# Performance work log

Hardware: AMD Instinct MI355X
Metric: run time of the kernel (lower is better)

The kernel has to match this reference:

```python
import jax, jax.numpy as jnp
import numpy as np

EMBED_DIM = 1024
BLOCK = 2048
HEAD = 64
BATCH = 4


def setup_inputs() -> dict:
    key = jax.random.key(0)
    k0, k1, k2, k3 = jax.random.split(key, 4)
    tokens = jax.random.normal(k0, (BATCH, BLOCK, EMBED_DIM), dtype=jnp.float32)
    # torch Linear(embed_dim, head_size, bias=False): init ~ U(-1/sqrt(in), 1/sqrt(in)).
    s = 1.0 / np.sqrt(EMBED_DIM)
    Wq = jax.random.uniform(k1, (EMBED_DIM, HEAD), jnp.float32, -s, s)
    Wk = jax.random.uniform(k2, (EMBED_DIM, HEAD), jnp.float32, -s, s)
    Wv = jax.random.uniform(k3, (EMBED_DIM, HEAD), jnp.float32, -s, s)
    return {"tokens": tokens, "Wq": Wq, "Wk": Wk, "Wv": Wv}


def reference(tokens, Wq, Wk, Wv):
    B, S, E = tokens.shape
    q = jnp.einsum('bse,eh->bsh', tokens, Wq)
    k = jnp.einsum('bse,eh->bsh', tokens, Wk)
    v = jnp.einsum('bse,eh->bsh', tokens, Wv)
    # NOTE: module scales by embed_dim**-0.5 (not head_size).
    wei = jnp.einsum('bqh,bkh->bqk', q, k) * (E ** -0.5)
    causal = jnp.tril(jnp.ones((S, S), dtype=bool))  # tril_mask[:block,:block]
    wei = jnp.where(causal, wei, -1e9)
    wei = jax.nn.softmax(wei, axis=-1)
    # dropout(p=0.3) is identity in eval mode (deterministic reference)
    return jnp.einsum('bqk,bkh->bqh', wei, v)
```

## Files before the change

### kernel.cpp

```cpp
#include <hip/hip_runtime.h>
#include <stdint.h>


typedef __bf16 bf16_t;
typedef __bf16 bf16x8 __attribute__((ext_vector_type(8)));
typedef __bf16 bf16x4 __attribute__((ext_vector_type(4)));
typedef float floatx4 __attribute__((ext_vector_type(4)));

#define MFMA16(a, b, c) __builtin_amdgcn_mfma_f32_16x16x32_bf16((a), (b), (c), 0, 0, 0)

static constexpr float kQScale = 0.04508422002778f;
#define NEG_BIG (-3.0e38f)

__device__ inline bf16x4 cvt4(float4 f) {
  bf16x4 v;
  v[0] = (bf16_t)f.x; v[1] = (bf16_t)f.y; v[2] = (bf16_t)f.z; v[3] = (bf16_t)f.w;
  return v;
}

__global__ __launch_bounds__(256) void wt_kernel(const float* __restrict__ Wq,
                                                 const float* __restrict__ Wk,
                                                 const float* __restrict__ Wv,
                                                 bf16_t* __restrict__ Bp) {
  const int tid = blockIdx.x * 256 + threadIdx.x;
  const int j = tid & 7;
  const int lane = (tid >> 3) & 63;
  const int ks = (tid >> 9) & 31;
  const int nt = tid >> 14;
  const int m = nt >> 2, n4 = nt & 3;
  const int h = n4 * 16 + (lane & 15);
  const int e = ks * 32 + ((lane >> 4) << 3) + j;
  const float* W = (m == 0) ? Wq : ((m == 1) ? Wk : Wv);
  float v = W[e * 64 + h];
  if (m == 0) v *= kQScale;
  Bp[tid] = (bf16_t)v;
}

__global__ __launch_bounds__(256) void proj_kernel(const float* __restrict__ tok,
                                                   const bf16_t* __restrict__ Bp,
                                                   bf16_t* __restrict__ qw,
                                                   bf16_t* __restrict__ kw,
                                                   bf16_t* __restrict__ vw) {
  __shared__ bf16_t As[2][16][264];
  const int tx = threadIdx.x;
  const int wave = tx >> 6, lane = tx & 63;
  const int lanelo = lane & 15, quad = lane >> 4;
  const int grow = blockIdx.x * 16;
  const int b = grow >> 11;
  const int t = (grow & 2047) >> 4;

  const float* tokbase = tok + (grow + wave) * 1024 + lane * 4;

  floatx4 acc[3];
#pragma unroll
  for (int i = 0; i < 3; i++) acc[i] = (floatx4){0.f, 0.f, 0.f, 0.f};

  const bf16_t* bp[3];
#pragma unroll
  for (int j = 0; j < 3; j++)
    bp[j] = Bp + (wave * 3 + j) * 16384 + lane * 8;

  float4 tb[4];
#pragma unroll
  for (int r = 0; r < 4; r++) tb[r] = *(const float4*)(tokbase + r * 4096);
#pragma unroll
  for (int r = 0; r < 4; r++)
    *(bf16x4*)&As[0][r * 4 + wave][lane * 4] = cvt4(tb[r]);
  __syncthreads();

  for (int c = 0; c < 4; c++) {
    if (c < 3) {
#pragma unroll
      for (int r = 0; r < 4; r++)
        tb[r] = *(const float4*)(tokbase + r * 4096 + (c + 1) * 256);
    }
    const bf16_t* ab = &As[c & 1][lanelo][quad * 8];
#pragma unroll
    for (int ks = 0; ks < 8; ks++) {
      const bf16x8 af = *(const bf16x8*)(ab + ks * 32);
#pragma unroll
      for (int j = 0; j < 3; j++) {
        const bf16x8 bfr = *(const bf16x8*)(bp[j] + (c * 8 + ks) * 512);
        acc[j] = MFMA16(af, bfr, acc[j]);
      }
    }
    if (c < 3) {
#pragma unroll
      for (int r = 0; r < 4; r++)
        *(bf16x4*)&As[(c + 1) & 1][r * 4 + wave][lane * 4] = cvt4(tb[r]);
    }
    __syncthreads();
  }

#pragma unroll
  for (int j = 0; j < 3; j++) {
    const int nt = wave * 3 + j;
    const int n4 = nt & 3, mtx = nt >> 2;
    const int h = n4 * 16 + lanelo;
    if (mtx < 2) {
      bf16_t* dst = (mtx == 0) ? qw : kw;
      const int ds = h >> 5;
      const int base = (((b * 128 + t) * 2 + ds) * 64 + (((h & 31) >> 3) << 4)) * 8 + (h & 7);
#pragma unroll
      for (int r = 0; r < 4; r++)
        dst[base + (quad * 4 + r) * 8] = (bf16_t)acc[j][r];
    } else {
#pragma unroll
      for (int r = 0; r < 4; r++) {
        const int ss = t * 16 + quad * 4 + r;
        const int c6 = ss >> 6, k6 = ss & 63;
        const int pos = ((k6 & 15) << 2) | (k6 >> 4);
        const int hh = pos >> 5, qv = (pos >> 3) & 3, jj = pos & 7;
        vw[((((b * 32 + c6) * 2 + hh) * 4 + n4) * 64 + qv * 16 + lanelo) * 8 + jj] =
            (bf16_t)acc[j][r];
      }
    }
  }
}

__global__ __launch_bounds__(512, 4) void attn_kernel(const bf16_t* __restrict__ qw,
                                                      const bf16_t* __restrict__ kw,
                                                      const bf16_t* __restrict__ vw,
                                                      float* __restrict__ out) {
  __shared__ float Ol[8][16][68];
  __shared__ float Ll[8][16];
  __shared__ bf16_t Pl[8][16 * 72];

  const int wave = threadIdx.x >> 6;
  const int lane = threadIdx.x & 63;
  const int lanelo = lane & 15;
  const int quad = lane >> 4;

  const int b = blockIdx.x & 3;
  const int t = 127 - (blockIdx.x >> 2);
  const int qbase = t * 16;
  const int grow = b * 2048 + qbase;

  const bf16_t* qp = qw + ((b * 128 + t) * 128 + lane) * 8;
  const bf16x8 qa0 = *(const bf16x8*)qp;
  const bf16x8 qa1 = *(const bf16x8*)(qp + 512);

  bf16x8 ones;
#pragma unroll
  for (int j = 0; j < 8; j++) ones[j] = (bf16_t)1.0f;

  floatx4 O[4];
#pragma unroll
  for (int i = 0; i < 4; i++) O[i] = (floatx4){0.f, 0.f, 0.f, 0.f};
  floatx4 lacc = (floatx4){0.f, 0.f, 0.f, 0.f};

  const int nch = (qbase + 16 + 63) >> 6;
  const int row0 = qbase + quad * 4;
  bf16_t* pw = &Pl[wave][0];
  const bf16_t* kb = kw + b * 131072 + lane * 8;
  const bf16_t* vb = vw + b * 131072 + lane * 8;

  for (int c = wave; c < nch; c += 8) {
    const int cb = c * 64;
    floatx4 s[4];
    const floatx4 z = (floatx4){0.f, 0.f, 0.f, 0.f};
#pragma unroll
    for (int sub = 0; sub < 4; sub++) {
      const bf16_t* kp = kb + (c * 4 + sub) * 1024;
      s[sub] = MFMA16(qa0, *(const bf16x8*)kp, z);
      s[sub] = MFMA16(qa1, *(const bf16x8*)(kp + 512), s[sub]);
    }

    if (cb + 63 > qbase) {
#pragma unroll
      for (int sub = 0; sub < 4; sub++) {
        const int key0 = cb + sub * 16 + lanelo;
#pragma unroll
        for (int r = 0; r < 4; r++)
          if (key0 > row0 + r) s[sub][r] = NEG_BIG;
      }
    }

    float p[4][4];
#pragma unroll
    for (int sub = 0; sub < 4; sub++)
#pragma unroll
      for (int r = 0; r < 4; r++)
        p[sub][r] = __builtin_amdgcn_exp2f(s[sub][r]);

    __builtin_amdgcn_wave_barrier();
#pragma unroll
    for (int r = 0; r < 4; r++) {
      bf16x4 pk;
      pk[0] = (bf16_t)p[0][r]; pk[1] = (bf16_t)p[1][r];
      pk[2] = (bf16_t)p[2][r]; pk[3] = (bf16_t)p[3][r];
      *(bf16x4*)&pw[(quad * 4 + r) * 72 + lanelo * 4] = pk;
    }
    __builtin_amdgcn_wave_barrier();
    const bf16_t* prd = pw + lanelo * 72 + quad * 8;
    const bf16x8 pa0 = *(const bf16x8*)prd;
    const bf16x8 pa1 = *(const bf16x8*)(prd + 32);
    __builtin_amdgcn_wave_barrier();

    const bf16_t* vp = vb + c * 4096;
#pragma unroll
    for (int dt = 0; dt < 4; dt++) {
      O[dt] = MFMA16(pa0, *(const bf16x8*)(vp + dt * 512), O[dt]);
      O[dt] = MFMA16(pa1, *(const bf16x8*)(vp + 2048 + dt * 512), O[dt]);
    }
    lacc = MFMA16(pa0, ones, lacc);
    lacc = MFMA16(pa1, ones, lacc);
  }

#pragma unroll
  for (int dt = 0; dt < 4; dt++)
#pragma unroll
    for (int r = 0; r < 4; r++)
      Ol[wave][quad * 4 + r][dt * 16 + lanelo] = O[dt][r];
  if (lanelo == 0) {
#pragma unroll
    for (int r = 0; r < 4; r++) Ll[wave][quad * 4 + r] = lacc[r];
  }
  __syncthreads();

#pragma unroll
  for (int o = threadIdx.x; o < 1024; o += 512) {
    const int row = o >> 6, d = o & 63;
    float L = 0.f, acc = 0.f;
#pragma unroll
    for (int w = 0; w < 8; w++) {
      L += Ll[w][row];
      acc += Ol[w][row][d];
    }
    out[(grow + row) * 64 + d] = acc / L;
  }
}

extern "C" void kernel_launch(void* const* d_in, const int* in_sizes, int n_in,
                              void* d_out, int out_size, void* d_ws, size_t ws_size,
                              hipStream_t stream) {
  const float* tokens = (const float*)d_in[0];
  const float* Wq = (const float*)d_in[1];
  const float* Wk = (const float*)d_in[2];
  const float* Wv = (const float*)d_in[3];
  float* out = (float*)d_out;

  char* ws = (char*)d_ws;
  if (ws_size < 3538944) return;
  bf16_t* Bp = (bf16_t*)ws;
  bf16_t* qw = (bf16_t*)(ws + 393216);
  bf16_t* kw = (bf16_t*)(ws + 393216 + 1048576);
  bf16_t* vw = (bf16_t*)(ws + 393216 + 2097152);

  hipLaunchKernelGGL(wt_kernel, dim3(768), dim3(256), 0, stream, Wq, Wk, Wv, Bp);
  hipLaunchKernelGGL(proj_kernel, dim3(512), dim3(256), 0, stream, tokens, Bp, qw, kw, vw);
  hipLaunchKernelGGL(attn_kernel, dim3(512), dim3(512), 0, stream, qw, kw, vw, out);
}
```

Baseline: 98.23 us.

## Transpose attention MFMAs to keep P in registers and stage projection stores via LDS

The attention kernel swaps the MFMA operand order so the score tile comes out transposed (keys along registers, queries along lanes). The exponentiated probabilities can then be packed straight into the B operand of the PV MFMA, with no LDS round trip or wave barriers. The causal mask, output staging and row-sum extraction are adjusted to the transposed layout. The projection kernel now stages Q/K through shared memory so they are written with coalesced 16-byte stores, and V is written as packed 4-element vectors under a revised layout.

```diff
diff --git a/kernel.cpp b/kernel.cpp
--- a/kernel.cpp
+++ b/kernel.cpp
@@ -92,29 +92,32 @@
     __syncthreads();
   }
 
+  bf16_t* Cs = (bf16_t*)As;
 #pragma unroll
   for (int j = 0; j < 3; j++) {
     const int nt = wave * 3 + j;
     const int n4 = nt & 3, mtx = nt >> 2;
-    const int h = n4 * 16 + lanelo;
     if (mtx < 2) {
-      bf16_t* dst = (mtx == 0) ? qw : kw;
-      const int ds = h >> 5;
-      const int base = (((b * 128 + t) * 2 + ds) * 64 + (((h & 31) >> 3) << 4)) * 8 + (h & 7);
 #pragma unroll
       for (int r = 0; r < 4; r++)
-        dst[base + (quad * 4 + r) * 8] = (bf16_t)acc[j][r];
+        Cs[(quad * 4 + r) * 136 + mtx * 64 + n4 * 16 + lanelo] = (bf16_t)acc[j][r];
     } else {
-#pragma unroll
-      for (int r = 0; r < 4; r++) {
-        const int ss = t * 16 + quad * 4 + r;
-        const int c6 = ss >> 6, k6 = ss & 63;
-        const int pos = ((k6 & 15) << 2) | (k6 >> 4);
-        const int hh = pos >> 5, qv = (pos >> 3) & 3, jj = pos & 7;
-        vw[((((b * 32 + c6) * 2 + hh) * 4 + n4) * 64 + qv * 16 + lanelo) * 8 + jj] =
-            (bf16_t)acc[j][r];
-      }
-    }
+      bf16x4 pk;
+#pragma unroll
+      for (int r = 0; r < 4; r++) pk[r] = (bf16_t)acc[j][r];
+      const int base = (((b * 32 + (t >> 2)) * 2 + ((t >> 1) & 1)) * 4 + n4) * 512
+                     + (quad * 16 + lanelo) * 8 + (t & 1) * 4;
+      *(bf16x4*)(vw + base) = pk;
+    }
+  }
+  __syncthreads();
+  {
+    const int mtx = tx >> 7, idx = tx & 127;
+    const int ds = idx >> 6, lp = idx & 63;
+    const int qr = lp & 15, h8 = ds * 32 + ((lp >> 4) << 3);
+    const bf16x8 val = *(const bf16x8*)&Cs[qr * 136 + mtx * 64 + h8];
+    bf16_t* dst = mtx ? kw : qw;
+    *(bf16x8*)(dst + (b * 128 + t) * 1024 + idx * 8) = val;
   }
 }
 
@@ -122,9 +125,8 @@
                                                       const bf16_t* __restrict__ kw,
                                                       const bf16_t* __restrict__ vw,
                                                       float* __restrict__ out) {
-  __shared__ float Ol[8][16][68];
+  __shared__ float Ol[8][16][65];
   __shared__ float Ll[8][16];
-  __shared__ bf16_t Pl[8][16 * 72];
 
   const int wave = threadIdx.x >> 6;
   const int lane = threadIdx.x & 63;
@@ -150,8 +152,6 @@
   floatx4 lacc = (floatx4){0.f, 0.f, 0.f, 0.f};
 
   const int nch = (qbase + 16 + 63) >> 6;
-  const int row0 = qbase + quad * 4;
-  bf16_t* pw = &Pl[wave][0];
   const bf16_t* kb = kw + b * 131072 + lane * 8;
   const bf16_t* vb = vw + b * 131072 + lane * 8;
 
@@ -162,60 +162,45 @@
 #pragma unroll
     for (int sub = 0; sub < 4; sub++) {
       const bf16_t* kp = kb + (c * 4 + sub) * 1024;
-      s[sub] = MFMA16(qa0, *(const bf16x8*)kp, z);
-      s[sub] = MFMA16(qa1, *(const bf16x8*)(kp + 512), s[sub]);
+      s[sub] = MFMA16(*(const bf16x8*)kp, qa0, z);
+      s[sub] = MFMA16(*(const bf16x8*)(kp + 512), qa1, s[sub]);
     }
 
     if (cb + 63 > qbase) {
 #pragma unroll
       for (int sub = 0; sub < 4; sub++) {
-        const int key0 = cb + sub * 16 + lanelo;
+        const int keyr = cb + sub * 16 + quad * 4;
 #pragma unroll
         for (int r = 0; r < 4; r++)
-          if (key0 > row0 + r) s[sub][r] = NEG_BIG;
+          if (keyr + r > qbase + lanelo) s[sub][r] = NEG_BIG;
       }
     }
 
-    float p[4][4];
-#pragma unroll
-    for (int sub = 0; sub < 4; sub++)
-#pragma unroll
-      for (int r = 0; r < 4; r++)
-        p[sub][r] = __builtin_amdgcn_exp2f(s[sub][r]);
-
-    __builtin_amdgcn_wave_barrier();
+    bf16x8 pa0, pa1;
 #pragma unroll
     for (int r = 0; r < 4; r++) {
-      bf16x4 pk;
-      pk[0] = (bf16_t)p[0][r]; pk[1] = (bf16_t)p[1][r];
-      pk[2] = (bf16_t)p[2][r]; pk[3] = (bf16_t)p[3][r];
-      *(bf16x4*)&pw[(quad * 4 + r) * 72 + lanelo * 4] = pk;
-    }
-    __builtin_amdgcn_wave_barrier();
-    const bf16_t* prd = pw + lanelo * 72 + quad * 8;
-    const bf16x8 pa0 = *(const bf16x8*)prd;
-    const bf16x8 pa1 = *(const bf16x8*)(prd + 32);
-    __builtin_amdgcn_wave_barrier();
+      pa0[r]     = (bf16_t)__builtin_amdgcn_exp2f(s[0][r]);
+      pa0[4 + r] = (bf16_t)__builtin_amdgcn_exp2f(s[1][r]);
+      pa1[r]     = (bf16_t)__builtin_amdgcn_exp2f(s[2][r]);
+      pa1[4 + r] = (bf16_t)__builtin_amdgcn_exp2f(s[3][r]);
+    }
 
     const bf16_t* vp = vb + c * 4096;
 #pragma unroll
     for (int dt = 0; dt < 4; dt++) {
-      O[dt] = MFMA16(pa0, *(const bf16x8*)(vp + dt * 512), O[dt]);
-      O[dt] = MFMA16(pa1, *(const bf16x8*)(vp + 2048 + dt * 512), O[dt]);
-    }
-    lacc = MFMA16(pa0, ones, lacc);
-    lacc = MFMA16(pa1, ones, lacc);
+      O[dt] = MFMA16(*(const bf16x8*)(vp + dt * 512), pa0, O[dt]);
+      O[dt] = MFMA16(*(const bf16x8*)(vp + 2048 + dt * 512), pa1, O[dt]);
+    }
+    lacc = MFMA16(ones, pa0, lacc);
+    lacc = MFMA16(ones, pa1, lacc);
   }
 
 #pragma unroll
   for (int dt = 0; dt < 4; dt++)
 #pragma unroll
     for (int r = 0; r < 4; r++)
-      Ol[wave][quad * 4 + r][dt * 16 + lanelo] = O[dt][r];
-  if (lanelo == 0) {
-#pragma unroll
-    for (int r = 0; r < 4; r++) Ll[wave][quad * 4 + r] = lacc[r];
-  }
+      Ol[wave][lanelo][dt * 16 + quad * 4 + r] = O[dt][r];
+  if (quad == 0) Ll[wave][lanelo] = lacc[0];
   __syncthreads();
 
 #pragma unroll
```

Measured after the change: 98.69 us. Within noise of the previous version (+0.5%).
